# Kernel optimization log

Measured on AMD Instinct MI355X. Metric: run time of the kernel, lower is better.

The kernel has to match this reference:

```python
import jax, jax.numpy as jnp
import numpy as np

STRIDE = 1
PADDING = 1


def setup_inputs() -> dict:
    key = jax.random.key(0)
    k1, k2, k3 = jax.random.split(key, 3)
    x = jax.random.normal(k1, (16, 64, 224, 224), dtype=jnp.float32)
    W = jax.random.normal(k2, (64, 64, 3, 3), dtype=jnp.float32)
    b = jax.random.normal(k3, (64,), dtype=jnp.float32)
    return {"x": x, "W": W, "b": b}


def reference(x, W, b):
    # Equivalent of the naive im2col+GEMM conv: a standard 2D convolution
    # (cross-correlation) with stride/padding, NCHW layout, OIHW weights.
    out = jax.lax.conv_general_dilated(
        x, W,
        window_strides=(STRIDE, STRIDE),
        padding=[(PADDING, PADDING), (PADDING, PADDING)],
        dimension_numbers=("NCHW", "OIHW", "NCHW"),
    )
    return out + b[None, :, None, None]
```

## Files before the change

kernel.cpp:

```cpp
#include <hip/hip_runtime.h>
#include <hip/hip_bf16.h>


typedef __attribute__((ext_vector_type(8)))  short   short8;
typedef __attribute__((ext_vector_type(8)))  unsigned short ushort8;
typedef __attribute__((ext_vector_type(16))) float   float16_t;

#define HW (224 * 224)

__device__ __forceinline__ unsigned short f2bf(float f) {
  __hip_bfloat16 h = __float2bfloat16(f);
  return *reinterpret_cast<unsigned short*>(&h);
}

__global__ void build_wt(const float* __restrict__ W, unsigned short* __restrict__ wt) {
  int i = blockIdx.x * 256 + threadIdx.x;
  if (i < 9 * 64 * 64) {
    int tap = i >> 12;
    int rem = i & 4095;
    int nn  = rem >> 6;
    int c   = rem & 63;
    wt[i] = f2bf(W[(nn * 64 + c) * 9 + tap]);
  }
}

__global__ __launch_bounds__(256, 2) void conv3x3_mfma(
    const float* __restrict__ x, const unsigned short* __restrict__ wt,
    const float* __restrict__ bias, float* __restrict__ out) {
  __shared__ __align__(16) unsigned short xs[18 * 8 * 34 * 8];

  const int bid = blockIdx.x;
  const int t   = (bid & 7) * 196 + (bid >> 3);
  const int bx  = t % 7;
  const int rem_t = t / 7;
  const int by  = rem_t % 14;
  const int img = rem_t / 14;

  const int w0  = bx * 32;
  const int h0  = by * 16;
  const int tid = threadIdx.x;
  const int lane = tid & 63, wave = tid >> 6;
  const int ln31 = lane & 31, lhi = lane >> 5;

  const float* xn = x + (size_t)img * 64 * HW;

  for (int i = tid; i < 18 * 8 * 34; i += 256) {
    int h   = i / (8 * 34);
    int rem = i - h * (8 * 34);
    int cg  = rem / 34;
    int w   = rem - cg * 34;
    int gh = h0 - 1 + h;
    int gw = w0 - 1 + w;
    ushort8 pk;
    if ((unsigned)gh < 224u && (unsigned)gw < 224u) {
      const float* p = xn + (size_t)cg * 8 * HW + gh * 224 + gw;
#pragma unroll
      for (int j = 0; j < 8; ++j) pk[j] = f2bf(p[(size_t)j * HW]);
    } else {
#pragma unroll
      for (int j = 0; j < 8; ++j) pk[j] = 0;
    }
    *reinterpret_cast<ushort8*>(&xs[i * 8]) = pk;
  }
  __syncthreads();

  const int row0 = wave * 4;
  float16_t acc[4][2];
#pragma unroll
  for (int rb = 0; rb < 4; ++rb)
#pragma unroll
    for (int nb = 0; nb < 2; ++nb) acc[rb][nb] = 0.f;

#pragma unroll
  for (int r = 0; r < 3; ++r) {
#pragma unroll
    for (int s = 0; s < 3; ++s) {
      const int tap = r * 3 + s;
      short8 bq[4][2];
#pragma unroll
      for (int ks = 0; ks < 4; ++ks)
#pragma unroll
        for (int nb = 0; nb < 2; ++nb)
          bq[ks][nb] = *reinterpret_cast<const short8*>(
              wt + ((tap * 64 + nb * 32 + ln31) * 64 + ks * 16 + lhi * 8));

#pragma unroll
      for (int ks = 0; ks < 4; ++ks) {
        const int cg = ks * 2 + lhi;
#pragma unroll
        for (int rb = 0; rb < 4; ++rb) {
          const int hidx = row0 + rb + r;
          const int widx = ln31 + s;
          const short8 a = *reinterpret_cast<const short8*>(
              &xs[(((hidx * 8) + cg) * 34 + widx) * 8]);
          acc[rb][0] = __builtin_amdgcn_mfma_f32_32x32x16_bf16(a, bq[ks][0], acc[rb][0], 0, 0, 0);
          acc[rb][1] = __builtin_amdgcn_mfma_f32_32x32x16_bf16(a, bq[ks][1], acc[rb][1], 0, 0, 0);
        }
      }
    }
  }

#pragma unroll
  for (int rb = 0; rb < 4; ++rb) {
    const int h = h0 + row0 + rb;
#pragma unroll
    for (int nb = 0; nb < 2; ++nb) {
      const int ch = nb * 32 + ln31;
      const float bv = bias[ch];
      float* op = out + (((size_t)img * 64 + ch) * 224 + h) * 224 + w0;
#pragma unroll
      for (int q = 0; q < 4; ++q) {
        const int wloc = 8 * q + 4 * lhi;
        float4 v;
        v.x = acc[rb][nb][4 * q + 0] + bv;
        v.y = acc[rb][nb][4 * q + 1] + bv;
        v.z = acc[rb][nb][4 * q + 2] + bv;
        v.w = acc[rb][nb][4 * q + 3] + bv;
        *reinterpret_cast<float4*>(op + wloc) = v;
      }
    }
  }
}

#define TW 32
#define TH 32
#define KB 16
#define PXT 4
__global__ __launch_bounds__(256) void conv3x3_direct(
    const float* __restrict__ x, const float* __restrict__ wgt,
    const float* __restrict__ bias, float* __restrict__ out) {
  __shared__ float xsf[34 * 35];
  const int tx = blockIdx.x % 7, ty = blockIdx.x / 7;
  const int k0 = blockIdx.y * KB, n = blockIdx.z;
  const int w0 = tx * TW, h0 = ty * TH;
  const int tid = threadIdx.x;
  const int tw = tid & 7, th = tid >> 3;
  float acc[KB][PXT];
#pragma unroll
  for (int k = 0; k < KB; ++k)
#pragma unroll
    for (int p = 0; p < PXT; ++p) acc[k][p] = 0.f;
  const float* xn = x + (size_t)n * 64 * HW;
  for (int c = 0; c < 64; ++c) {
    const float* xc = xn + (size_t)c * HW;
    for (int i = tid; i < 34 * 34; i += 256) {
      int row = i / 34, col = i - row * 34;
      int gh = h0 - 1 + row, gw = w0 - 1 + col;
      float v = 0.f;
      if (gh >= 0 && gh < 224 && gw >= 0 && gw < 224) v = xc[gh * 224 + gw];
      xsf[row * 35 + col] = v;
    }
    __syncthreads();
    float in[3][6];
#pragma unroll
    for (int r = 0; r < 3; ++r)
#pragma unroll
      for (int q = 0; q < 6; ++q) in[r][q] = xsf[(th + r) * 35 + tw * PXT + q];
    const float* wc = wgt + ((size_t)k0 * 64 + c) * 9;
#pragma unroll
    for (int k = 0; k < KB; ++k) {
      const float* wk = wc + (size_t)k * 64 * 9;
#pragma unroll
      for (int r = 0; r < 3; ++r)
#pragma unroll
        for (int s = 0; s < 3; ++s) {
          float wv = wk[r * 3 + s];
#pragma unroll
          for (int p = 0; p < PXT; ++p) acc[k][p] += wv * in[r][s + p];
        }
    }
    __syncthreads();
  }
#pragma unroll
  for (int k = 0; k < KB; ++k) {
    float bv = bias[k0 + k];
    float4 v = make_float4(acc[k][0] + bv, acc[k][1] + bv, acc[k][2] + bv, acc[k][3] + bv);
    float* op = out + ((((size_t)n * 64 + (k0 + k)) * 224 + (h0 + th)) * 224 + (w0 + tw * PXT));
    *reinterpret_cast<float4*>(op) = v;
  }
}

extern "C" void kernel_launch(void* const* d_in, const int* in_sizes, int n_in,
                              void* d_out, int out_size, void* d_ws, size_t ws_size,
                              hipStream_t stream) {
  const float* x = (const float*)d_in[0];
  const float* W = (const float*)d_in[1];
  const float* b = (const float*)d_in[2];
  float* out = (float*)d_out;

  if (ws_size >= 9 * 64 * 64 * sizeof(unsigned short)) {
    unsigned short* wt = (unsigned short*)d_ws;
    build_wt<<<144, 256, 0, stream>>>(W, wt);
    conv3x3_mfma<<<1568, 256, 0, stream>>>(x, wt, b, out);
  } else {
    dim3 grid(7 * 7, 64 / KB, 16);
    conv3x3_direct<<<grid, 256, 0, stream>>>(x, W, b, out);
  }
}
```

Measured before the change: 462.2 us.

## Use 512-thread blocks with two rows per wave and batched staging loads

Doubles the block to 8 waves, each computing 2 output rows instead of 4, which halves the accumulator registers per wave and raises occupancy through launch bounds (512,4). The global-to-LDS staging loop now issues loads for three items before converting and storing them, giving more memory-level parallelism. In exchange, each wave reloads the weight fragments for fewer MFMAs, so weight reuse per wave drops, and the higher register pressure target could cause spills.

```diff
diff --git a/kernel.cpp b/kernel.cpp
--- a/kernel.cpp
+++ b/kernel.cpp
@@ -24,7 +24,7 @@
   }
 }
 
-__global__ __launch_bounds__(256, 2) void conv3x3_mfma(
+__global__ __launch_bounds__(512, 4) void conv3x3_mfma(
     const float* __restrict__ x, const unsigned short* __restrict__ wt,
     const float* __restrict__ bias, float* __restrict__ out) {
   __shared__ __align__(16) unsigned short xs[18 * 8 * 34 * 8];
@@ -44,30 +44,47 @@
 
   const float* xn = x + (size_t)img * 64 * HW;
 
-  for (int i = tid; i < 18 * 8 * 34; i += 256) {
-    int h   = i / (8 * 34);
-    int rem = i - h * (8 * 34);
-    int cg  = rem / 34;
-    int w   = rem - cg * 34;
-    int gh = h0 - 1 + h;
-    int gw = w0 - 1 + w;
-    ushort8 pk;
-    if ((unsigned)gh < 224u && (unsigned)gw < 224u) {
-      const float* p = xn + (size_t)cg * 8 * HW + gh * 224 + gw;
-#pragma unroll
-      for (int j = 0; j < 8; ++j) pk[j] = f2bf(p[(size_t)j * HW]);
-    } else {
-#pragma unroll
-      for (int j = 0; j < 8; ++j) pk[j] = 0;
-    }
-    *reinterpret_cast<ushort8*>(&xs[i * 8]) = pk;
+  const int NITEMS = 18 * 8 * 34;
+  for (int base = tid; base < NITEMS; base += 512 * 3) {
+    float va[3][8];
+    int   iw[3];
+#pragma unroll
+    for (int it = 0; it < 3; ++it) {
+      const int i = base + it * 512;
+      iw[it] = i;
+      if (i < NITEMS) {
+        const int h   = i / (8 * 34);
+        const int rem = i - h * (8 * 34);
+        const int cg  = rem / 34;
+        const int w   = rem - cg * 34;
+        const int gh  = h0 - 1 + h;
+        const int gw  = w0 - 1 + w;
+        if (((unsigned)gh < 224u) && ((unsigned)gw < 224u)) {
+          const float* p = xn + (size_t)cg * 8 * HW + gh * 224 + gw;
+#pragma unroll
+          for (int j = 0; j < 8; ++j) va[it][j] = p[(size_t)j * HW];
+        } else {
+#pragma unroll
+          for (int j = 0; j < 8; ++j) va[it][j] = 0.f;
+        }
+      }
+    }
+#pragma unroll
+    for (int it = 0; it < 3; ++it) {
+      if (iw[it] < NITEMS) {
+        ushort8 pk;
+#pragma unroll
+        for (int j = 0; j < 8; ++j) pk[j] = f2bf(va[it][j]);
+        *reinterpret_cast<ushort8*>(&xs[iw[it] * 8]) = pk;
+      }
+    }
   }
   __syncthreads();
 
-  const int row0 = wave * 4;
-  float16_t acc[4][2];
-#pragma unroll
-  for (int rb = 0; rb < 4; ++rb)
+  const int row0 = wave * 2;
+  float16_t acc[2][2];
+#pragma unroll
+  for (int rb = 0; rb < 2; ++rb)
 #pragma unroll
     for (int nb = 0; nb < 2; ++nb) acc[rb][nb] = 0.f;
 
@@ -88,7 +105,7 @@
       for (int ks = 0; ks < 4; ++ks) {
         const int cg = ks * 2 + lhi;
 #pragma unroll
-        for (int rb = 0; rb < 4; ++rb) {
+        for (int rb = 0; rb < 2; ++rb) {
           const int hidx = row0 + rb + r;
           const int widx = ln31 + s;
           const short8 a = *reinterpret_cast<const short8*>(
@@ -101,7 +118,7 @@
   }
 
 #pragma unroll
-  for (int rb = 0; rb < 4; ++rb) {
+  for (int rb = 0; rb < 2; ++rb) {
     const int h = h0 + row0 + rb;
 #pragma unroll
     for (int nb = 0; nb < 2; ++nb) {
@@ -191,7 +208,7 @@
   if (ws_size >= 9 * 64 * 64 * sizeof(unsigned short)) {
     unsigned short* wt = (unsigned short*)d_ws;
     build_wt<<<144, 256, 0, stream>>>(W, wt);
-    conv3x3_mfma<<<1568, 256, 0, stream>>>(x, wt, b, out);
+    conv3x3_mfma<<<1568, 512, 0, stream>>>(x, wt, b, out);
   } else {
     dim3 grid(7 * 7, 64 / KB, 16);
     conv3x3_direct<<<grid, 256, 0, stream>>>(x, W, b, out);
```

Result: slower. 487.1 us (+5.4%).

## Pre-pack input to NHWC bf16 and use direct-to-LDS loads in conv kernel

Applied to the files above, without the earlier changes.

Adds a pre-pass that converts the NCHW fp32 input to an NHWC bf16 workspace. A new conv kernel then stages 4-row by 114-pixel strips into LDS with global_load_lds and an XOR swizzle, and computes two output rows per block with MFMA. The goal is to replace the strided, channel-gathering fp32 loads and in-kernel conversion with contiguous 16-byte loads and less halo redundancy. In exchange it adds a full extra read and write of the input through a large workspace (about 100 MB), and it only runs when the workspace is big enough.

```diff
diff --git a/kernel.cpp b/kernel.cpp
--- a/kernel.cpp
+++ b/kernel.cpp
@@ -7,6 +7,9 @@
 typedef __attribute__((ext_vector_type(16))) float   float16_t;
 
 #define HW (224 * 224)
+
+typedef __attribute__((address_space(1))) const void gas_void;
+typedef __attribute__((address_space(3))) void las_void;
 
 __device__ __forceinline__ unsigned short f2bf(float f) {
   __hip_bfloat16 h = __float2bfloat16(f);
@@ -24,27 +27,149 @@
   }
 }
 
-__global__ __launch_bounds__(256, 2) void conv3x3_mfma(
+__global__ __launch_bounds__(256, 4) void pack_xt(
+    const float* __restrict__ x, unsigned short* __restrict__ xt) {
+  const int n = blockIdx.x / 196;
+  const int p = (blockIdx.x - n * 196) * 256 + threadIdx.x;
+  const float* xp = x + (size_t)n * 64 * HW + p;
+  unsigned short* op = xt + ((size_t)n * HW + p) * 64;
+#pragma unroll
+  for (int c0 = 0; c0 < 64; c0 += 8) {
+    float v[8];
+#pragma unroll
+    for (int j = 0; j < 8; ++j) v[j] = xp[(size_t)(c0 + j) * HW];
+    ushort8 pk;
+#pragma unroll
+    for (int j = 0; j < 8; ++j) pk[j] = f2bf(v[j]);
+    *reinterpret_cast<ushort8*>(op + c0) = pk;
+  }
+}
+
+__global__ __launch_bounds__(448, 3) void conv3x3_nhwc(
+    const unsigned short* __restrict__ xt, const unsigned short* __restrict__ wt,
+    const float* __restrict__ bias, float* __restrict__ out) {
+  __shared__ __align__(16) unsigned short xs[4 * 114 * 64];
+
+  const int bid = blockIdx.x;
+  const int t   = (bid & 7) * 448 + (bid >> 3);
+  const int wb2 = t & 1;
+  const int rest = t >> 1;
+  const int ht  = rest % 112;
+  const int img = rest / 112;
+  const int h0  = ht * 2;
+  const int wb  = wb2 * 112;
+
+  const int tid = threadIdx.x;
+  const int lane = tid & 63, wave = tid >> 6;
+  const int ln31 = lane & 31, lhi = lane >> 5;
+
+  const unsigned short* xti = xt + (size_t)img * HW * 64;
+
+  const int lds_px0 = wb2 ? 0 : 1;
+  const int gw_ch0  = wb2 ? 111 : 0;
+  const int pxl  = lane >> 3;
+  const int slot = lane & 7;
+  for (int c = wave; c < 56; c += 7) {
+    const int r  = c / 14;
+    const int ch = c - r * 14;
+    const int gh = h0 - 1 + r;
+    const int base_px = r * 114 + lds_px0 + ch * 8;
+    unsigned short* lbase = &xs[(size_t)base_px * 64];
+    if ((unsigned)gh < 224u) {
+      const int lpx = base_px + pxl;
+      const int gp  = gw_ch0 + ch * 8 + pxl;
+      const unsigned short* gsrc = xti + ((size_t)(gh * 224 + gp)) * 64
+                                       + (size_t)((slot ^ (lpx & 7)) * 8);
+      __builtin_amdgcn_global_load_lds((gas_void*)gsrc, (las_void*)lbase, 16, 0, 0);
+    } else {
+      uint4 z = make_uint4(0u, 0u, 0u, 0u);
+      *reinterpret_cast<uint4*>(&xs[(size_t)base_px * 64 + (size_t)lane * 8]) = z;
+    }
+  }
+  if (tid < 64) {
+    const int r     = tid >> 4;
+    const int which = (tid >> 3) & 1;
+    const int sl    = tid & 7;
+    const int col   = which ? (wb2 ? 112 : 113) : (wb2 ? 113 : 0);
+    const int gwT   = wb2 ? 223 : 112;
+    const int gh    = h0 - 1 + r;
+    const int lin   = r * 114 + col;
+    unsigned short* dst = &xs[(size_t)lin * 64 + (size_t)((sl ^ (lin & 7)) * 8)];
+    uint4 v = make_uint4(0u, 0u, 0u, 0u);
+    if (which && ((unsigned)gh < 224u)) {
+      v = *reinterpret_cast<const uint4*>(
+          xti + ((size_t)(gh * 224 + gwT)) * 64 + (size_t)sl * 8);
+    }
+    *reinterpret_cast<uint4*>(dst) = v;
+  }
+  __syncthreads();
+
+  const int p    = wave * 32 + ln31;
+  const int orow = (p >= 112) ? 1 : 0;
+  const int ocol = p - orow * 112;
+
+  float16_t acc[2];
+  acc[0] = 0.f; acc[1] = 0.f;
+
+#pragma unroll
+  for (int ks = 0; ks < 4; ++ks) {
+    const int sl = ks * 2 + lhi;
+#pragma unroll
+    for (int r = 0; r < 3; ++r) {
+#pragma unroll
+      for (int s = 0; s < 3; ++s) {
+        const int tap = r * 3 + s;
+        const short8 b0 = *reinterpret_cast<const short8*>(
+            wt + ((tap * 64 + ln31) * 64 + ks * 16 + lhi * 8));
+        const short8 b1 = *reinterpret_cast<const short8*>(
+            wt + ((tap * 64 + 32 + ln31) * 64 + ks * 16 + lhi * 8));
+        const int lin = (orow + r) * 114 + (ocol + s);
+        const short8 a = *reinterpret_cast<const short8*>(
+            &xs[(size_t)lin * 64 + (size_t)((sl ^ (lin & 7)) * 8)]);
+        acc[0] = __builtin_amdgcn_mfma_f32_32x32x16_bf16(a, b0, acc[0], 0, 0, 0);
+        acc[1] = __builtin_amdgcn_mfma_f32_32x32x16_bf16(a, b1, acc[1], 0, 0, 0);
+      }
+    }
+  }
+
+#pragma unroll
+  for (int nb = 0; nb < 2; ++nb) {
+    const int chn = nb * 32 + ln31;
+    const float bv = bias[chn];
+    float* ob = out + ((size_t)img * 64 + chn) * (size_t)HW;
+#pragma unroll
+    for (int q = 0; q < 4; ++q) {
+      const int m   = 8 * q + 4 * lhi;
+      const int pix = wave * 32 + m;
+      const int r2  = (pix >= 112) ? 1 : 0;
+      const int cc  = pix - r2 * 112;
+      float4 v;
+      v.x = acc[nb][4 * q + 0] + bv;
+      v.y = acc[nb][4 * q + 1] + bv;
+      v.z = acc[nb][4 * q + 2] + bv;
+      v.w = acc[nb][4 * q + 3] + bv;
+      *reinterpret_cast<float4*>(ob + (size_t)(h0 + r2) * 224 + wb + cc) = v;
+    }
+  }
+}
+
+__global__ __launch_bounds__(256, 2) void conv3x3_mfma_tile(
     const float* __restrict__ x, const unsigned short* __restrict__ wt,
     const float* __restrict__ bias, float* __restrict__ out) {
   __shared__ __align__(16) unsigned short xs[18 * 8 * 34 * 8];
-
   const int bid = blockIdx.x;
   const int t   = (bid & 7) * 196 + (bid >> 3);
   const int bx  = t % 7;
   const int rem_t = t / 7;
   const int by  = rem_t % 14;
   const int img = rem_t / 14;
-
   const int w0  = bx * 32;
   const int h0  = by * 16;
   const int tid = threadIdx.x;
   const int lane = tid & 63, wave = tid >> 6;
   const int ln31 = lane & 31, lhi = lane >> 5;
-
   const float* xn = x + (size_t)img * 64 * HW;
-
-  for (int i = tid; i < 18 * 8 * 34; i += 256) {
+  for (int i = tid; i < 18 * 8 * 10 * 0 + 18 * 8 * 34; i += 256) {
     int h   = i / (8 * 34);
     int rem = i - h * (8 * 34);
     int cg  = rem / 34;
@@ -53,9 +178,9 @@
     int gw = w0 - 1 + w;
     ushort8 pk;
     if ((unsigned)gh < 224u && (unsigned)gw < 224u) {
-      const float* p = xn + (size_t)cg * 8 * HW + gh * 224 + gw;
-#pragma unroll
-      for (int j = 0; j < 8; ++j) pk[j] = f2bf(p[(size_t)j * HW]);
+      const float* pp = xn + (size_t)cg * 8 * HW + gh * 224 + gw;
+#pragma unroll
+      for (int j = 0; j < 8; ++j) pk[j] = f2bf(pp[(size_t)j * HW]);
     } else {
 #pragma unroll
       for (int j = 0; j < 8; ++j) pk[j] = 0;
@@ -63,14 +188,12 @@
     *reinterpret_cast<ushort8*>(&xs[i * 8]) = pk;
   }
   __syncthreads();
-
   const int row0 = wave * 4;
   float16_t acc[4][2];
 #pragma unroll
   for (int rb = 0; rb < 4; ++rb)
 #pragma unroll
     for (int nb = 0; nb < 2; ++nb) acc[rb][nb] = 0.f;
-
 #pragma unroll
   for (int r = 0; r < 3; ++r) {
 #pragma unroll
@@ -83,7 +206,6 @@
         for (int nb = 0; nb < 2; ++nb)
           bq[ks][nb] = *reinterpret_cast<const short8*>(
               wt + ((tap * 64 + nb * 32 + ln31) * 64 + ks * 16 + lhi * 8));
-
 #pragma unroll
       for (int ks = 0; ks < 4; ++ks) {
         const int cg = ks * 2 + lhi;
@@ -99,7 +221,6 @@
       }
     }
   }
-
 #pragma unroll
   for (int rb = 0; rb < 4; ++rb) {
     const int h = h0 + row0 + rb;
@@ -188,10 +309,19 @@
   const float* b = (const float*)d_in[2];
   float* out = (float*)d_out;
 
-  if (ws_size >= 9 * 64 * 64 * sizeof(unsigned short)) {
+  const size_t WT_BYTES = (size_t)9 * 64 * 64 * sizeof(unsigned short);
+  const size_t XT_BYTES = (size_t)16 * HW * 64 * sizeof(unsigned short);
+
+  if (ws_size >= WT_BYTES + XT_BYTES) {
+    unsigned short* wt = (unsigned short*)d_ws;
+    unsigned short* xt = (unsigned short*)((char*)d_ws + WT_BYTES);
+    build_wt<<<144, 256, 0, stream>>>(W, wt);
+    pack_xt<<<16 * 196, 256, 0, stream>>>(x, xt);
+    conv3x3_nhwc<<<3584, 448, 0, stream>>>(xt, wt, b, out);
+  } else if (ws_size >= WT_BYTES) {
     unsigned short* wt = (unsigned short*)d_ws;
     build_wt<<<144, 256, 0, stream>>>(W, wt);
-    conv3x3_mfma<<<1568, 256, 0, stream>>>(x, wt, b, out);
+    conv3x3_mfma_tile<<<1568, 256, 0, stream>>>(x, wt, b, out);
   } else {
     dim3 grid(7 * 7, 64 / KB, 16);
     conv3x3_direct<<<grid, 256, 0, stream>>>(x, W, b, out);
```

Result: slower. 601.5 us (+30.1%).
